# Kernel optimization log

Hardware: AMD Instinct MI355X
Metric: run time of the kernel (lower is better)

The kernel has to match this reference:

```python
import jax, jax.numpy as jnp
import numpy as np

B, H, S, D, HID = 2, 4, 512, 16, 32

def setup_inputs() -> dict:
    key = jax.random.key(0)
    ks = jax.random.split(key, 12)
    sc = 1.0 / np.sqrt(D)
    return {
        "v": jax.random.normal(ks[0], (B, H, S, D), jnp.float32),
        "k": jax.random.normal(ks[1], (B, H, S, D), jnp.float32),
        "q": jax.random.normal(ks[2], (B, H, S, D), jnp.float32),
        "mask": jnp.zeros((B, 1, S, S), jnp.float32),
        "Wq": jax.random.normal(ks[3], (D, D), jnp.float32) * sc,
        "bq": jnp.zeros((D,), jnp.float32),
        "Wk": jax.random.normal(ks[4], (D, D), jnp.float32) * sc,
        "bk": jnp.zeros((D,), jnp.float32),
        "Wv": jax.random.normal(ks[5], (D, D), jnp.float32) * sc,
        "bv": jnp.zeros((D,), jnp.float32),
        "Wo": jax.random.normal(ks[6], (D, D), jnp.float32) * sc,
        "bo": jnp.zeros((D,), jnp.float32),
        "N1": jax.random.normal(ks[7], (2 * D, HID), jnp.float32) * (1.0 / np.sqrt(2 * D)),
        "b1": jnp.zeros((HID,), jnp.float32),
        "N2": jax.random.normal(ks[8], (HID, 1), jnp.float32) * (1.0 / np.sqrt(HID)),
        "b2": jnp.zeros((1,), jnp.float32),
    }

def _pair_mlp_scores(qh, kh, N1, b1, N2, b2):
    # NN(concat(q_i, k_j)) computed without materializing the 2*D concat:
    # first layer = q_i @ N1[:D] + k_j @ N1[D:] + b1, broadcast-summed over pairs.
    d = qh.shape[-1]
    A, Bm = N1[:d], N1[d:]
    hq = jnp.einsum("bhsd,df->bhsf", qh, A)   # (B,H,Sq,HID)
    hk = jnp.einsum("bhsd,df->bhsf", kh, Bm)  # (B,H,Sk,HID)
    pre = hq[:, :, :, None, :] + hk[:, :, None, :, :] + b1  # (B,H,Sq,Sk,HID)
    return jnp.einsum("bhqkf,fo->bhqk", jax.nn.relu(pre), N2[:, :]) + b2[0]

def reference(v, k, q, mask, Wq, bq, Wk, bk, Wv, bv, Wo, bo, N1, b1, N2, b2):
    qp = q @ Wq + bq
    kp = k @ Wk + bk
    vp = v @ Wv + bv
    logits = _pair_mlp_scores(qp, kp, N1, b1, N2, b2)
    # make_sym=True: add NN(concat(k_j, q_i))
    logits = logits + _pair_mlp_scores(kp, qp, N1, b1, N2, b2).swapaxes(-1, -2)
    logits = logits + mask * -1e9
    attn = jax.nn.softmax(logits, axis=-1)          # (B,H,Sq,Sk)
    out = jnp.einsum("bhqk,bhkd->bhqd", attn, vp)   # (B,H,Sq,D)
    return out @ Wo + bo, attn
```

## Files before the change

### kernel.cpp

```cpp
#include <hip/hip_runtime.h>

#define NB 2
#define NH 4
#define NS 512
#define ND 16
#define NF 32

typedef float v2f __attribute__((ext_vector_type(2)));


__global__ __launch_bounds__(256) void k_proj(
    const float* __restrict__ q, const float* __restrict__ kin, const float* __restrict__ v,
    const float* __restrict__ Wq, const float* __restrict__ bq,
    const float* __restrict__ Wk, const float* __restrict__ bk,
    const float* __restrict__ Wv, const float* __restrict__ bv,
    const float* __restrict__ N1, const float* __restrict__ b1,
    float* __restrict__ hq, float* __restrict__ hk, float* __restrict__ vpt)
{
    __shared__ float m_s[16 * 32];
    __shared__ float c_s[32];

    const int bid = blockIdx.x;
    const int job = bid % 5;
    const int sc  = (bid / 5) & 1;
    const int bh  = bid / 10;
    const int t   = threadIdx.x;

    const float* W    = (job < 2) ? Wq : (job < 4 ? Wk : Wv);
    const float* bias = (job < 2) ? bq : (job < 4 ? bk : bv);
    const float* x    = (job < 2) ? q  : (job < 4 ? kin : v);

    if (job < 4) {
        const int noff = (job & 1) * 16;
        for (int i = t; i < 512; i += 256) {
            int e = i >> 5, f = i & 31;
            float m = 0.f;
#pragma unroll
            for (int d = 0; d < 16; ++d)
                m = fmaf(W[e * 16 + d], N1[(noff + d) * 32 + f], m);
            m_s[i] = m;
        }
        if (t < 32) {
            float c = (job & 1) ? b1[t] : 0.f;
#pragma unroll
            for (int d = 0; d < 16; ++d)
                c = fmaf(bias[d], N1[(noff + d) * 32 + t], c);
            c_s[t] = c;
        }
    } else {
        int e = t >> 4, d = t & 15;
        m_s[e * 32 + d] = W[e * 16 + d];
        if (t < 16) c_s[t] = bias[t];
    }
    __syncthreads();

    const int s = sc * 256 + t;
    const int r = bh * NS + s;

    float xv[16];
    const float4* x4 = (const float4*)(x + (size_t)r * 16);
#pragma unroll
    for (int j = 0; j < 4; ++j) {
        float4 a = x4[j];
        xv[4*j] = a.x; xv[4*j+1] = a.y; xv[4*j+2] = a.z; xv[4*j+3] = a.w;
    }

    if (job < 4) {
        float* outb = ((job < 2) ? hq : hk) + (size_t)bh * 32768 + (size_t)(job & 1) * 16384;
        float h[32];
#pragma unroll
        for (int f = 0; f < 32; ++f) h[f] = c_s[f];
#pragma unroll
        for (int e = 0; e < 16; ++e)
#pragma unroll
            for (int f = 0; f < 32; ++f)
                h[f] = fmaf(xv[e], m_s[e * 32 + f], h[f]);
#pragma unroll
        for (int f = 0; f < 32; ++f)
            outb[(size_t)f * NS + s] = h[f];
    } else {
        float* outb = vpt + (size_t)bh * 8192;
        float h[16];
#pragma unroll
        for (int d = 0; d < 16; ++d) h[d] = c_s[d];
#pragma unroll
        for (int e = 0; e < 16; ++e)
#pragma unroll
            for (int d = 0; d < 16; ++d)
                h[d] = fmaf(xv[e], m_s[e * 32 + d], h[d]);
#pragma unroll
        for (int d = 0; d < 16; ++d)
            outb[(size_t)d * NS + s] = h[d];
    }
}

__global__ __launch_bounds__(512, 4) void k_fused(
    const float* __restrict__ hq, const float* __restrict__ hk,
    const float* __restrict__ vpt,
    const float* __restrict__ N2, const float* __restrict__ b2,
    const float* __restrict__ mask,
    const float* __restrict__ Wo, const float* __restrict__ bo,
    float* __restrict__ attn, float* __restrict__ out)
{
    __shared__ __align__(16) float hq_s[8 * 68];
    __shared__ __align__(16) float attn_s[8 * 516];
    __shared__ float wo_s[256];
    __shared__ float bo_s[16];
    __shared__ float ov_s[128];
    __shared__ float part_s[128 * 17];
    __shared__ float redm[64];
    __shared__ float reds[64];

    const int bh  = blockIdx.x >> 6;
    const int q0  = (blockIdx.x & 63) << 3;
    const int tid = threadIdx.x;
    const int wave = tid >> 6, lane = tid & 63;
    const int k = tid;
    const size_t base = (size_t)bh * 32768;

    v2f hk2A[16], hk2B[16], n2v[16];
#pragma unroll
    for (int f2 = 0; f2 < 16; ++f2) {
        hk2A[f2] = (v2f){ hk[base + (size_t)(2*f2    ) * NS + k],
                          hk[base + (size_t)(2*f2 + 1) * NS + k] };
        hk2B[f2] = (v2f){ hk[base + (size_t)(32 + 2*f2) * NS + k],
                          hk[base + (size_t)(33 + 2*f2) * NS + k] };
        n2v[f2]  = (v2f){ N2[2*f2], N2[2*f2 + 1] };
    }
    const float b2v = 2.0f * b2[0];
    const float* mbase = mask + (size_t)(bh >> 2) * NS * NS;

    {
        int f = tid >> 3, qi = tid & 7;
        hq_s[qi * 68 + f] = hq[base + (size_t)f * NS + q0 + qi];
    }
    if (tid < 256) wo_s[tid] = Wo[tid];
    if (tid < 16)  bo_s[tid] = bo[tid];
    __syncthreads();

    float sreg[8];
    float mnext = mbase[(size_t)q0 * NS + k];
#pragma unroll
    for (int qi = 0; qi < 8; ++qi) {
        float mcur = mnext;
        if (qi < 7) mnext = mbase[(size_t)(q0 + qi + 1) * NS + k];
        const v2f* hq2 = (const v2f*)(hq_s + qi * 68);
        v2f acc_a = 0.f, acc_b = 0.f;
        const v2f z = 0.f;
#pragma unroll
        for (int f2 = 0; f2 < 16; ++f2) {
            v2f t1 = hq2[f2]      + hk2B[f2];
            v2f t2 = hq2[16 + f2] + hk2A[f2];
            v2f r  = __builtin_elementwise_max(t1, z) + __builtin_elementwise_max(t2, z);
            if (f2 & 1) acc_b += n2v[f2] * r;
            else        acc_a += n2v[f2] * r;
        }
        v2f av = acc_a + acc_b;
        float s = av.x + av.y + b2v;
        s = fmaf(mcur, -1e9f, s);
        sreg[qi] = s;

        float m = s;
#pragma unroll
        for (int off = 32; off > 0; off >>= 1) m = fmaxf(m, __shfl_xor(m, off));
        if (lane == 0) redm[qi * 8 + wave] = m;
    }
    __syncthreads();

#pragma unroll
    for (int qi = 0; qi < 8; ++qi) {
        float bm = redm[qi * 8];
#pragma unroll
        for (int w = 1; w < 8; ++w) bm = fmaxf(bm, redm[qi * 8 + w]);
        float sm = sreg[qi] - bm;
        sreg[qi] = sm;
        float e = __expf(sm);
        float ss = e;
#pragma unroll
        for (int off = 32; off > 0; off >>= 1) ss += __shfl_xor(ss, off);
        if (lane == 0) reds[qi * 8 + wave] = ss;
    }
    __syncthreads();

#pragma unroll
    for (int qi = 0; qi < 8; ++qi) {
        float tot = reds[qi * 8];
#pragma unroll
        for (int w = 1; w < 8; ++w) tot += reds[qi * 8 + w];
        float p = __expf(sreg[qi]) / tot;
        attn[(size_t)(bh * NS + q0 + qi) * NS + k] = p;
        attn_s[qi * 516 + k] = p;
    }
    __syncthreads();

    {
        const int qi_p = tid & 7;
        const int dgrp = (tid >> 3) & 3;
        const int koct = tid >> 5;
        const float4* a4 = (const float4*)attn_s;
        const float4* v4 = (const float4*)(vpt + (size_t)bh * 8192);
        float acc0 = 0.f, acc1 = 0.f, acc2 = 0.f, acc3 = 0.f;
#pragma unroll
        for (int kq = 0; kq < 8; ++kq) {
            const int k4 = koct * 8 + kq;
            float4 av = a4[qi_p * 129 + k4];
            float4 w0 = v4[(dgrp * 4 + 0) * 128 + k4];
            float4 w1 = v4[(dgrp * 4 + 1) * 128 + k4];
            float4 w2 = v4[(dgrp * 4 + 2) * 128 + k4];
            float4 w3 = v4[(dgrp * 4 + 3) * 128 + k4];
            acc0 = fmaf(av.x, w0.x, fmaf(av.y, w0.y, fmaf(av.z, w0.z, fmaf(av.w, w0.w, acc0))));
            acc1 = fmaf(av.x, w1.x, fmaf(av.y, w1.y, fmaf(av.z, w1.z, fmaf(av.w, w1.w, acc1))));
            acc2 = fmaf(av.x, w2.x, fmaf(av.y, w2.y, fmaf(av.z, w2.z, fmaf(av.w, w2.w, acc2))));
            acc3 = fmaf(av.x, w3.x, fmaf(av.y, w3.y, fmaf(av.z, w3.z, fmaf(av.w, w3.w, acc3))));
        }
        part_s[(qi_p * 16 + dgrp * 4 + 0) * 17 + koct] = acc0;
        part_s[(qi_p * 16 + dgrp * 4 + 1) * 17 + koct] = acc1;
        part_s[(qi_p * 16 + dgrp * 4 + 2) * 17 + koct] = acc2;
        part_s[(qi_p * 16 + dgrp * 4 + 3) * 17 + koct] = acc3;
    }
    __syncthreads();

    if (tid < 128) {
        float ov = 0.f;
#pragma unroll
        for (int kh = 0; kh < 16; ++kh) ov += part_s[tid * 17 + kh];
        ov_s[tid] = ov;
    }
    __syncthreads();

    if (tid < 128) {
        const int qi2 = tid >> 4, d = tid & 15;
        float res = bo_s[d];
#pragma unroll
        for (int e = 0; e < 16; ++e)
            res = fmaf(ov_s[qi2 * 16 + e], wo_s[e * 16 + d], res);
        out[(size_t)(bh * NS + q0 + qi2) * 16 + d] = res;
    }
}

extern "C" void kernel_launch(void* const* d_in, const int* in_sizes, int n_in,
                              void* d_out, int out_size, void* d_ws, size_t ws_size,
                              hipStream_t stream)
{
    const float* v    = (const float*)d_in[0];
    const float* k    = (const float*)d_in[1];
    const float* q    = (const float*)d_in[2];
    const float* mask = (const float*)d_in[3];
    const float* Wq   = (const float*)d_in[4];
    const float* bq   = (const float*)d_in[5];
    const float* Wk   = (const float*)d_in[6];
    const float* bk   = (const float*)d_in[7];
    const float* Wv   = (const float*)d_in[8];
    const float* bv   = (const float*)d_in[9];
    const float* Wo   = (const float*)d_in[10];
    const float* bo   = (const float*)d_in[11];
    const float* N1   = (const float*)d_in[12];
    const float* b1   = (const float*)d_in[13];
    const float* N2   = (const float*)d_in[14];
    const float* b2   = (const float*)d_in[15];

    float* out  = (float*)d_out;
    float* attn = out + (size_t)NB*NH*NS*ND;

    float* hq  = (float*)d_ws;
    float* hk  = hq + (size_t)8 * 32768;
    float* vpt = hk + (size_t)8 * 32768;

    k_proj <<<80, 256, 0, stream>>>(q, k, v, Wq, bq, Wk, bk, Wv, bv, N1, b1, hq, hk, vpt);
    k_fused<<<512, 512, 0, stream>>>(hq, hk, vpt, N2, b2, mask, Wo, bo, attn, out);
}
```

Before: 34.49 us.

## Store hq row-major and read it directly from global in fused kernel

The projection kernel now transposes hq through shared memory and writes it row-major (64 floats per query row), so the fused kernel can read each query's hidden vector as uniform, contiguous global loads instead of staging a strided gather into shared memory. The fused kernel also keeps the softmax exponentials in registers rather than recomputing exp in the normalization pass. In exchange, k_proj gains a large shared buffer and an extra barrier, and the fused kernel's hq reads now go to global or scalar cache instead of LDS.

```diff
diff --git a/kernel.cpp b/kernel.cpp
--- a/kernel.cpp
+++ b/kernel.cpp
@@ -15,10 +15,11 @@
     const float* __restrict__ Wk, const float* __restrict__ bk,
     const float* __restrict__ Wv, const float* __restrict__ bv,
     const float* __restrict__ N1, const float* __restrict__ b1,
-    float* __restrict__ hq, float* __restrict__ hk, float* __restrict__ vpt)
+    float* __restrict__ hq_rm, float* __restrict__ hk, float* __restrict__ vpt)
 {
     __shared__ float m_s[16 * 32];
     __shared__ float c_s[32];
+    __shared__ float trans_s[256 * 33];
 
     const int bid = blockIdx.x;
     const int job = bid % 5;
@@ -65,8 +66,27 @@
         xv[4*j] = a.x; xv[4*j+1] = a.y; xv[4*j+2] = a.z; xv[4*j+3] = a.w;
     }
 
-    if (job < 4) {
-        float* outb = ((job < 2) ? hq : hk) + (size_t)bh * 32768 + (size_t)(job & 1) * 16384;
+    if (job < 2) {
+        float h[32];
+#pragma unroll
+        for (int f = 0; f < 32; ++f) h[f] = c_s[f];
+#pragma unroll
+        for (int e = 0; e < 16; ++e)
+#pragma unroll
+            for (int f = 0; f < 32; ++f)
+                h[f] = fmaf(xv[e], m_s[e * 32 + f], h[f]);
+#pragma unroll
+        for (int f = 0; f < 32; ++f) trans_s[t * 33 + f] = h[f];
+        __syncthreads();
+        float* outb = hq_rm + (((size_t)(bh * NS + sc * 256)) << 6) + (job & 1) * 32;
+#pragma unroll
+        for (int it = 0; it < 32; ++it) {
+            int j = it * 256 + t;
+            int sl = j >> 5, f = j & 31;
+            outb[((size_t)sl << 6) + f] = trans_s[sl * 33 + f];
+        }
+    } else if (job < 4) {
+        float* outb = hk + (size_t)bh * 32768 + (size_t)(job & 1) * 16384;
         float h[32];
 #pragma unroll
         for (int f = 0; f < 32; ++f) h[f] = c_s[f];
@@ -95,14 +115,13 @@
 }
 
 __global__ __launch_bounds__(512, 4) void k_fused(
-    const float* __restrict__ hq, const float* __restrict__ hk,
+    const float* __restrict__ hq_rm, const float* __restrict__ hk,
     const float* __restrict__ vpt,
     const float* __restrict__ N2, const float* __restrict__ b2,
     const float* __restrict__ mask,
     const float* __restrict__ Wo, const float* __restrict__ bo,
     float* __restrict__ attn, float* __restrict__ out)
 {
-    __shared__ __align__(16) float hq_s[8 * 68];
     __shared__ __align__(16) float attn_s[8 * 516];
     __shared__ float wo_s[256];
     __shared__ float bo_s[16];
@@ -130,10 +149,6 @@
     const float b2v = 2.0f * b2[0];
     const float* mbase = mask + (size_t)(bh >> 2) * NS * NS;
 
-    {
-        int f = tid >> 3, qi = tid & 7;
-        hq_s[qi * 68 + f] = hq[base + (size_t)f * NS + q0 + qi];
-    }
     if (tid < 256) wo_s[tid] = Wo[tid];
     if (tid < 16)  bo_s[tid] = bo[tid];
     __syncthreads();
@@ -144,7 +159,7 @@
     for (int qi = 0; qi < 8; ++qi) {
         float mcur = mnext;
         if (qi < 7) mnext = mbase[(size_t)(q0 + qi + 1) * NS + k];
-        const v2f* hq2 = (const v2f*)(hq_s + qi * 68);
+        const v2f* hq2 = (const v2f*)(hq_rm + (((size_t)(bh * NS + q0 + qi)) << 6));
         v2f acc_a = 0.f, acc_b = 0.f;
         const v2f z = 0.f;
 #pragma unroll
@@ -167,14 +182,14 @@
     }
     __syncthreads();
 
+    float preg[8];
 #pragma unroll
     for (int qi = 0; qi < 8; ++qi) {
         float bm = redm[qi * 8];
 #pragma unroll
         for (int w = 1; w < 8; ++w) bm = fmaxf(bm, redm[qi * 8 + w]);
-        float sm = sreg[qi] - bm;
-        sreg[qi] = sm;
-        float e = __expf(sm);
+        float e = __expf(sreg[qi] - bm);
+        preg[qi] = e;
         float ss = e;
 #pragma unroll
         for (int off = 32; off > 0; off >>= 1) ss += __shfl_xor(ss, off);
@@ -187,7 +202,7 @@
         float tot = reds[qi * 8];
 #pragma unroll
         for (int w = 1; w < 8; ++w) tot += reds[qi * 8 + w];
-        float p = __expf(sreg[qi]) / tot;
+        float p = preg[qi] / tot;
         attn[(size_t)(bh * NS + q0 + qi) * NS + k] = p;
         attn_s[qi * 516 + k] = p;
     }
@@ -262,10 +277,10 @@
     float* out  = (float*)d_out;
     float* attn = out + (size_t)NB*NH*NS*ND;
 
-    float* hq  = (float*)d_ws;
-    float* hk  = hq + (size_t)8 * 32768;
-    float* vpt = hk + (size_t)8 * 32768;
-
-    k_proj <<<80, 256, 0, stream>>>(q, k, v, Wq, bq, Wk, bk, Wv, bv, N1, b1, hq, hk, vpt);
-    k_fused<<<512, 512, 0, stream>>>(hq, hk, vpt, N2, b2, mask, Wo, bo, attn, out);
+    float* hq_rm = (float*)d_ws;
+    float* hk    = hq_rm + (size_t)8 * 32768;
+    float* vpt   = hk + (size_t)8 * 32768;
+
+    k_proj <<<80, 256, 0, stream>>>(q, k, v, Wq, bq, Wk, bk, Wv, bv, N1, b1, hq_rm, hk, vpt);
+    k_fused<<<512, 512, 0, stream>>>(hq_rm, hk, vpt, N2, b2, mask, Wo, bo, attn, out);
 }
```

Result: faster. 32.96 us (-4.4%).
